# Kernel tuning notes

Measured on AMD Instinct MI355X. Metric: run time of the kernel, lower is better.

Reference implementation:

```python
import jax, jax.numpy as jnp
import numpy as np

B, S, E, L, H, FF, CB = 16, 1000, 512, 4, 8, 2048, 4096
DH = E // H

def _ln(x, g, b):
    m = x.mean(-1, keepdims=True)
    v = ((x - m) ** 2).mean(-1, keepdims=True)
    return (x - m) / jnp.sqrt(v + 1e-5) * g + b

def setup_inputs() -> dict:
    key = jax.random.key(0)
    cnt = [0]
    def rn(shape, s=0.02):
        cnt[0] += 1
        return jax.random.normal(jax.random.fold_in(key, cnt[0]), shape, jnp.float32) * s
    inp = {}
    inp['noisy_tokens'] = jax.random.randint(jax.random.fold_in(key, 999), (B, S), 0, CB, dtype=jnp.int32)
    inp['codebook'] = rn((CB, E), 1.0)
    # sinusoidal positional encoding, as in _create_positional_encoding
    pe = np.zeros((S, E), np.float32)
    pos = np.arange(S, dtype=np.float32)[:, None]
    div = np.exp(np.arange(0, E, 2, dtype=np.float32) * (-np.log(10000.0) / E))
    pe[:, 0::2] = np.sin(pos * div)
    pe[:, 1::2] = np.cos(pos * div)
    inp['pos_enc'] = jnp.asarray(pe)[None]  # [1,S,E]
    # transformer encoder layers (stacked over L)
    inp['qkv_w'] = rn((L, 3 * E, E)); inp['qkv_b'] = jnp.zeros((L, 3 * E))
    inp['out_w'] = rn((L, E, E));     inp['out_b'] = jnp.zeros((L, E))
    inp['ln1_g'] = jnp.ones((L, E));  inp['ln1_b'] = jnp.zeros((L, E))
    inp['ln2_g'] = jnp.ones((L, E));  inp['ln2_b'] = jnp.zeros((L, E))
    inp['ff1_w'] = rn((L, FF, E));    inp['ff1_b'] = jnp.zeros((L, FF))
    inp['ff2_w'] = rn((L, E, FF));    inp['ff2_b'] = jnp.zeros((L, E))
    inp['fin_g'] = jnp.ones((E,));    inp['fin_b'] = jnp.zeros((E,))
    # post_process: Linear, LN, GELU, Linear
    inp['pp1_w'] = rn((E, E)); inp['pp1_b'] = jnp.zeros((E,))
    inp['pp_ln_g'] = jnp.ones((E,)); inp['pp_ln_b'] = jnp.zeros((E,))
    inp['pp2_w'] = rn((E, E)); inp['pp2_b'] = jnp.zeros((E,))
    inp['res_w'] = jnp.float32(0.1)
    # feature_to_codebook: Linear, LN, GELU, Linear (codebook_dim == E)
    inp['fc1_w'] = rn((E, E)); inp['fc1_b'] = jnp.zeros((E,))
    inp['fc_ln_g'] = jnp.ones((E,)); inp['fc_ln_b'] = jnp.zeros((E,))
    inp['fc2_w'] = rn((E, E)); inp['fc2_b'] = jnp.zeros((E,))
    return inp

def reference(noisy_tokens, codebook, pos_enc, qkv_w, qkv_b, out_w, out_b,
              ln1_g, ln1_b, ln2_g, ln2_b, ff1_w, ff1_b, ff2_w, ff2_b,
              fin_g, fin_b, pp1_w, pp1_b, pp_ln_g, pp_ln_b, pp2_w, pp2_b,
              res_w, fc1_w, fc1_b, fc_ln_g, fc_ln_b, fc2_w, fc2_b):
    gelu = lambda z: jax.nn.gelu(z, approximate=False)
    # token embedding (codebook_projection is Identity) + positional encoding
    x = codebook[noisy_tokens] + pos_enc            # [B,S,E]
    # pre-norm transformer encoder (dropout=0 / eval)
    y = x
    for l in range(L):
        h = _ln(y, ln1_g[l], ln1_b[l])
        qkv = h @ qkv_w[l].T + qkv_b[l]             # [B,S,3E]
        q, k, v = jnp.split(qkv, 3, axis=-1)
        q = q.reshape(B, S, H, DH); k = k.reshape(B, S, H, DH); v = v.reshape(B, S, H, DH)
        scores = jnp.einsum('bqhd,bkhd->bhqk', q, k) / jnp.sqrt(jnp.float32(DH))
        attn = jax.nn.softmax(scores, axis=-1)
        ctx = jnp.einsum('bhqk,bkhd->bqhd', attn, v).reshape(B, S, E)
        y = y + (ctx @ out_w[l].T + out_b[l])
        h2 = _ln(y, ln2_g[l], ln2_b[l])
        y = y + (gelu(h2 @ ff1_w[l].T + ff1_b[l]) @ ff2_w[l].T + ff2_b[l])
    y = _ln(y, fin_g, fin_b)
    # post_process + residual
    pp = gelu(_ln(y @ pp1_w.T + pp1_b, pp_ln_g, pp_ln_b)) @ pp2_w.T + pp2_b
    enhanced = x + res_w * pp
    # feature_to_codebook
    fc = gelu(_ln(enhanced @ fc1_w.T + fc1_b, fc_ln_g, fc_ln_b)) @ fc2_w.T + fc2_b  # [B,S,E]
    # quantize: nearest neighbour in codebook (cdist + argmin)
    flat = fc.reshape(-1, E)
    d2 = (jnp.sum(flat ** 2, -1, keepdims=True)
          - 2.0 * flat @ codebook.T
          + jnp.sum(codebook ** 2, -1))            # [B*S, CB]
    tokens = jnp.argmin(d2, axis=-1).reshape(B, S)
    return fc, tokens
```

## Files before the change

### kernel.cpp

```cpp
#include <hip/hip_runtime.h>
#include <hip/hip_bf16.h>
#include <math.h>

#define NTOK 16000
#define E    512
#define FFD  2048
#define CBN  4096
#define SEQ  1000
#define NH   8
#define VLD  1008

typedef __hip_bfloat16 bf16;
typedef __attribute__((ext_vector_type(8))) short short8;
typedef __attribute__((ext_vector_type(4))) float f32x4;

__device__ __forceinline__ float gelu_f(float v) {
    return 0.5f * v * (1.0f + erff(v * 0.70710678118654752f));
}

__device__ __forceinline__ void split_store(float v, bf16* hi, bf16* lo, size_t idx) {
    bf16 h = __float2bfloat16(v);
    hi[idx] = h;
    lo[idx] = __float2bfloat16(v - __bfloat162float(h));
}

__device__ __forceinline__ void t2_ins(float v, int c, float& v1, int& c1, float& v2, int& c2) {
    const bool b1 = (v < v1) || (v == v1 && c < c1);
    const bool b2 = (v < v2) || (v == v2 && c < c2);
    if (b1) { v2 = v1; c2 = c1; v1 = v; c1 = c; }
    else if (b2) { v2 = v; c2 = c; }
}

__global__ __launch_bounds__(128) void embed_kernel(const int* __restrict__ tok,
                                                    const float* __restrict__ cb,
                                                    const float* __restrict__ pe,
                                                    float* __restrict__ y) {
    const int row = blockIdx.x;
    const int s = row % SEQ;
    const int t = tok[row];
    const int c = threadIdx.x * 4;
    const float4 cv = *(const float4*)(cb + (size_t)t * E + c);
    const float4 pv = *(const float4*)(pe + (size_t)s * E + c);
    *(float4*)(y + (size_t)row * E + c) =
        make_float4(cv.x + pv.x, cv.y + pv.y, cv.z + pv.z, cv.w + pv.w);
}

__global__ __launch_bounds__(256) void split_w(const float* __restrict__ src, int ld,
                                               int cols_log2, int n,
                                               bf16* __restrict__ hi, bf16* __restrict__ lo) {
    const int i = blockIdx.x * 256 + threadIdx.x;
    if (i >= n) return;
    const int r = i >> cols_log2;
    const int c = i & ((1 << cols_log2) - 1);
    const float v = src[(size_t)r * ld + c];
    split_store(v, hi, lo, i);
}

template<int GELU>
__global__ __launch_bounds__(256) void ln_planes(const float* __restrict__ in,
                                                 bf16* __restrict__ hi, bf16* __restrict__ lo,
                                                 const float* __restrict__ g,
                                                 const float* __restrict__ b) {
    const int lane = threadIdx.x & 63;
    const int row = blockIdx.x * 4 + (threadIdx.x >> 6);
    const float* p = in + (size_t)row * E;
    const float4 v0 = *(const float4*)(p + lane * 4);
    const float4 v1 = *(const float4*)(p + 256 + lane * 4);
    float sum = v0.x + v0.y + v0.z + v0.w + v1.x + v1.y + v1.z + v1.w;
    float sq = v0.x * v0.x + v0.y * v0.y + v0.z * v0.z + v0.w * v0.w
             + v1.x * v1.x + v1.y * v1.y + v1.z * v1.z + v1.w * v1.w;
#pragma unroll
    for (int m = 1; m < 64; m <<= 1) {
        sum += __shfl_xor(sum, m);
        sq += __shfl_xor(sq, m);
    }
    const float mean = sum * (1.0f / 512.0f);
    const float var = sq * (1.0f / 512.0f) - mean * mean;
    const float rstd = rsqrtf(var + 1e-5f);
    const float4 g0 = *(const float4*)(g + lane * 4);
    const float4 g1 = *(const float4*)(g + 256 + lane * 4);
    const float4 b0 = *(const float4*)(b + lane * 4);
    const float4 b1 = *(const float4*)(b + 256 + lane * 4);
    const size_t base = (size_t)row * E;
    float o;
    const float vv0[4] = {v0.x, v0.y, v0.z, v0.w};
    const float gg0[4] = {g0.x, g0.y, g0.z, g0.w};
    const float bb0[4] = {b0.x, b0.y, b0.z, b0.w};
    const float vv1[4] = {v1.x, v1.y, v1.z, v1.w};
    const float gg1[4] = {g1.x, g1.y, g1.z, g1.w};
    const float bb1[4] = {b1.x, b1.y, b1.z, b1.w};
#pragma unroll
    for (int t = 0; t < 4; ++t) {
        o = (vv0[t] - mean) * rstd * gg0[t] + bb0[t];
        if (GELU) o = gelu_f(o);
        split_store(o, hi, lo, base + lane * 4 + t);
        o = (vv1[t] - mean) * rstd * gg1[t] + bb1[t];
        if (GELU) o = gelu_f(o);
        split_store(o, hi, lo, base + 256 + lane * 4 + t);
    }
}

template<int OUT>
__global__ __launch_bounds__(256) void gemm_split(
    const bf16* __restrict__ Ah, const bf16* __restrict__ Al, int lda,
    const bf16* __restrict__ Wh, const bf16* __restrict__ Wl, int ldw,
    const float* __restrict__ bias,
    float* __restrict__ C, int ldc,
    bf16* __restrict__ Ohi, bf16* __restrict__ Olo, int ldp,
    const int* __restrict__ noisy, const float* __restrict__ cb,
    const float* __restrict__ pe, const float* __restrict__ resw,
    int K) {
    __shared__ short Ash[2][128][40];
    __shared__ short Wsh[2][128][40];
    const int tid = threadIdx.x;
    const int rowBase = blockIdx.y * 128;
    const int colBase = blockIdx.x * 128;
    const int wave = tid >> 6, lane = tid & 63;
    const int wm = (wave & 1) * 64, wn = (wave >> 1) * 64;
    const int lm = lane & 15;
    const int q8 = (lane >> 4) * 8;
    const int r0 = tid >> 2;
    const int kq = (tid & 3) * 8;

    f32x4 acc[4][4];
#pragma unroll
    for (int i = 0; i < 4; ++i)
#pragma unroll
        for (int j = 0; j < 4; ++j)
            acc[i][j] = (f32x4){0.f, 0.f, 0.f, 0.f};

    for (int k0 = 0; k0 < K; k0 += 32) {
        __syncthreads();
        {
            const size_t a0 = (size_t)(rowBase + r0) * lda + k0 + kq;
            const size_t a1 = (size_t)(rowBase + r0 + 64) * lda + k0 + kq;
            const size_t w0 = (size_t)(colBase + r0) * ldw + k0 + kq;
            const size_t w1 = (size_t)(colBase + r0 + 64) * ldw + k0 + kq;
            *(short8*)&Ash[0][r0][kq]      = *(const short8*)(Ah + a0);
            *(short8*)&Ash[0][r0 + 64][kq] = *(const short8*)(Ah + a1);
            *(short8*)&Ash[1][r0][kq]      = *(const short8*)(Al + a0);
            *(short8*)&Ash[1][r0 + 64][kq] = *(const short8*)(Al + a1);
            *(short8*)&Wsh[0][r0][kq]      = *(const short8*)(Wh + w0);
            *(short8*)&Wsh[0][r0 + 64][kq] = *(const short8*)(Wh + w1);
            *(short8*)&Wsh[1][r0][kq]      = *(const short8*)(Wl + w0);
            *(short8*)&Wsh[1][r0 + 64][kq] = *(const short8*)(Wl + w1);
        }
        __syncthreads();
        short8 ah[4], al[4], wh[4], wl[4];
#pragma unroll
        for (int i = 0; i < 4; ++i) {
            ah[i] = *(const short8*)&Ash[0][wm + i * 16 + lm][q8];
            al[i] = *(const short8*)&Ash[1][wm + i * 16 + lm][q8];
            wh[i] = *(const short8*)&Wsh[0][wn + i * 16 + lm][q8];
            wl[i] = *(const short8*)&Wsh[1][wn + i * 16 + lm][q8];
        }
#pragma unroll
        for (int i = 0; i < 4; ++i)
#pragma unroll
            for (int j = 0; j < 4; ++j)
                acc[i][j] = __builtin_amdgcn_mfma_f32_16x16x32_bf16(ah[i], wh[j], acc[i][j], 0, 0, 0);
#pragma unroll
        for (int i = 0; i < 4; ++i)
#pragma unroll
            for (int j = 0; j < 4; ++j)
                acc[i][j] = __builtin_amdgcn_mfma_f32_16x16x32_bf16(ah[i], wl[j], acc[i][j], 0, 0, 0);
#pragma unroll
        for (int i = 0; i < 4; ++i)
#pragma unroll
            for (int j = 0; j < 4; ++j)
                acc[i][j] = __builtin_amdgcn_mfma_f32_16x16x32_bf16(al[i], wh[j], acc[i][j], 0, 0, 0);
    }

    float bv[4];
#pragma unroll
    for (int j = 0; j < 4; ++j)
        bv[j] = bias ? bias[colBase + wn + j * 16 + lm] : 0.f;
    float scv = 0.f;
    if (OUT == 3) scv = resw[0];
#pragma unroll
    for (int i = 0; i < 4; ++i) {
#pragma unroll
        for (int reg = 0; reg < 4; ++reg) {
            const int r = rowBase + wm + i * 16 + (lane >> 4) * 4 + reg;
            int tok = 0, srow = 0;
            if (OUT == 3) { tok = noisy[r]; srow = r % SEQ; }
#pragma unroll
            for (int j = 0; j < 4; ++j) {
                const int col = colBase + wn + j * 16 + lm;
                float v = acc[i][j][reg] + bv[j];
                if (OUT == 0) {
                    C[(size_t)r * ldc + col] = v;
                } else if (OUT == 1) {
                    float* cp = C + (size_t)r * ldc + col;
                    *cp = *cp + v;
                } else if (OUT == 2) {
                    v = gelu_f(v);
                    split_store(v, Ohi, Olo, (size_t)r * ldp + col);
                } else if (OUT == 3) {
                    const float xv = cb[(size_t)tok * E + col] + pe[(size_t)srow * E + col];
                    v = xv + scv * v;
                    split_store(v, Ohi, Olo, (size_t)r * ldp + col);
                } else {
                    split_store(v, Ohi, Olo, (size_t)r * ldp + col);
                }
            }
        }
    }
}

__global__ __launch_bounds__(256) void vtrans(const bf16* __restrict__ vh_src,
                                              const bf16* __restrict__ vl_src,
                                              bf16* __restrict__ vth,
                                              bf16* __restrict__ vtl) {
    __shared__ short T[64][72];
    const int tid = threadIdx.x;
    const int st = blockIdx.x;
    const int bh = blockIdx.y;
    const int b = bh >> 3, h = bh & 7;
    const int sr = tid >> 2, dq = (tid & 3) * 16;
    const int s_g = st * 64 + sr;
    const int od = tid >> 3;
    const int osq = (tid & 7) * 8;
#pragma unroll
    for (int p = 0; p < 2; ++p) {
        const short* src = (const short*)(p ? vl_src : vh_src);
        short* dst = (short*)(p ? vtl : vth);
        short8 a0 = {0, 0, 0, 0, 0, 0, 0, 0};
        short8 a1 = {0, 0, 0, 0, 0, 0, 0, 0};
        if (s_g < SEQ) {
            const short* sp = src + (size_t)(b * SEQ + s_g) * 1536 + 1024 + h * 64 + dq;
            a0 = *(const short8*)sp;
            a1 = *(const short8*)(sp + 8);
        }
        __syncthreads();
#pragma unroll
        for (int j = 0; j < 8; ++j) T[dq + j][sr] = a0[j];
#pragma unroll
        for (int j = 0; j < 8; ++j) T[dq + 8 + j][sr] = a1[j];
        __syncthreads();
        const int scol = st * 64 + osq;
        if (scol + 8 <= VLD) {
            const short8 o0 = *(const short8*)&T[od][osq];
            const short8 o1 = *(const short8*)&T[od + 32][osq];
            *(short8*)(dst + (size_t)(bh * 64 + od) * VLD + scol) = o0;
            *(short8*)(dst + (size_t)(bh * 64 + od + 32) * VLD + scol) = o1;
        }
    }
}

__global__ __launch_bounds__(256) void attn_mfma(const bf16* __restrict__ qkh,
                                                 const bf16* __restrict__ qkl,
                                                 const bf16* __restrict__ vth,
                                                 const bf16* __restrict__ vtl,
                                                 bf16* __restrict__ chi,
                                                 bf16* __restrict__ clo) {
    __shared__ short QPs[2][64][72];
    __shared__ short Ks[2][64][72];
    __shared__ short Vs[2][64][72];
    const int tid = threadIdx.x;
    const int qt = blockIdx.x, bh = blockIdx.y;
    const int b = bh >> 3, h = bh & 7;
    const int wave = tid >> 6, lane = tid & 63;
    const int lm = lane & 15, g = lane >> 4, q8 = g * 8;
    const int wq = wave * 16;
    const int r0 = tid >> 2, kq = (tid & 3) * 16;

    {
        const int q = qt * 64 + r0;
        short8 z = {0, 0, 0, 0, 0, 0, 0, 0};
        short8 a0 = z, a1 = z, b0 = z, b1 = z;
        if (q < SEQ) {
            const size_t base = (size_t)(b * SEQ + q) * 1536 + h * 64 + kq;
            a0 = *(const short8*)((const short*)qkh + base);
            a1 = *(const short8*)((const short*)qkh + base + 8);
            b0 = *(const short8*)((const short*)qkl + base);
            b1 = *(const short8*)((const short*)qkl + base + 8);
        }
        *(short8*)&QPs[0][r0][kq] = a0; *(short8*)&QPs[0][r0][kq + 8] = a1;
        *(short8*)&QPs[1][r0][kq] = b0; *(short8*)&QPs[1][r0][kq + 8] = b1;
    }
    __syncthreads();
    short8 qfh[2], qfl[2];
#pragma unroll
    for (int t = 0; t < 2; ++t) {
        qfh[t] = *(const short8*)&QPs[0][wq + lm][t * 32 + q8];
        qfl[t] = *(const short8*)&QPs[1][wq + lm][t * 32 + q8];
    }

    float m_i[4] = {-3e38f, -3e38f, -3e38f, -3e38f};
    float l_i[4] = {0.f, 0.f, 0.f, 0.f};
    f32x4 o[4];
#pragma unroll
    for (int dt = 0; dt < 4; ++dt) o[dt] = (f32x4){0.f, 0.f, 0.f, 0.f};

    for (int kb = 0; kb < SEQ; kb += 64) {
        __syncthreads();
        {
            const int kr = kb + r0;
            short8 z = {0, 0, 0, 0, 0, 0, 0, 0};
            short8 a0 = z, a1 = z, b0 = z, b1 = z;
            if (kr < SEQ) {
                const size_t base = (size_t)(b * SEQ + kr) * 1536 + 512 + h * 64 + kq;
                a0 = *(const short8*)((const short*)qkh + base);
                a1 = *(const short8*)((const short*)qkh + base + 8);
                b0 = *(const short8*)((const short*)qkl + base);
                b1 = *(const short8*)((const short*)qkl + base + 8);
            }
            *(short8*)&Ks[0][r0][kq] = a0; *(short8*)&Ks[0][r0][kq + 8] = a1;
            *(short8*)&Ks[1][r0][kq] = b0; *(short8*)&Ks[1][r0][kq + 8] = b1;
            const size_t vbase = (size_t)(bh * 64 + r0) * VLD + kb + kq;
            short8 v0 = z, v1 = z, w0 = z, w1 = z;
            if (kb + kq + 8 <= VLD) {
                v0 = *(const short8*)((const short*)vth + vbase);
                w0 = *(const short8*)((const short*)vtl + vbase);
            }
            if (kb + kq + 16 <= VLD) {
                v1 = *(const short8*)((const short*)vth + vbase + 8);
                w1 = *(const short8*)((const short*)vtl + vbase + 8);
            }
            *(short8*)&Vs[0][r0][kq] = v0; *(short8*)&Vs[0][r0][kq + 8] = v1;
            *(short8*)&Vs[1][r0][kq] = w0; *(short8*)&Vs[1][r0][kq + 8] = w1;
        }
        __syncthreads();
        f32x4 sac[4];
#pragma unroll
        for (int j = 0; j < 4; ++j) sac[j] = (f32x4){0.f, 0.f, 0.f, 0.f};
#pragma unroll
        for (int t = 0; t < 2; ++t) {
#pragma unroll
            for (int j = 0; j < 4; ++j) {
                const short8 kh = *(const short8*)&Ks[0][j * 16 + lm][t * 32 + q8];
                const short8 kl = *(const short8*)&Ks[1][j * 16 + lm][t * 32 + q8];
                sac[j] = __builtin_amdgcn_mfma_f32_16x16x32_bf16(qfh[t], kh, sac[j], 0, 0, 0);
                sac[j] = __builtin_amdgcn_mfma_f32_16x16x32_bf16(qfh[t], kl, sac[j], 0, 0, 0);
                sac[j] = __builtin_amdgcn_mfma_f32_16x16x32_bf16(qfl[t], kh, sac[j], 0, 0, 0);
            }
        }
        float alpha_v[4];
#pragma unroll
        for (int reg = 0; reg < 4; ++reg) {
            float sv[4];
            float rm = -3e38f;
#pragma unroll
            for (int j = 0; j < 4; ++j) {
                const int kc = kb + j * 16 + lm;
                float s = sac[j][reg] * 0.125f;
                s = (kc < SEQ) ? s : -3e38f;
                sv[j] = s;
                rm = fmaxf(rm, s);
            }
#pragma unroll
            for (int m = 1; m < 16; m <<= 1) rm = fmaxf(rm, __shfl_xor(rm, m));
            const float mn = fmaxf(m_i[reg], rm);
            const float al = expf(m_i[reg] - mn);
            float rs = 0.f;
            const int prow = wq + g * 4 + reg;
#pragma unroll
            for (int j = 0; j < 4; ++j) {
                const float pv = expf(sv[j] - mn);
                rs += pv;
                bf16 phb = __float2bfloat16(pv);
                bf16 plb = __float2bfloat16(pv - __bfloat162float(phb));
                QPs[0][prow][j * 16 + lm] = *reinterpret_cast<short*>(&phb);
                QPs[1][prow][j * 16 + lm] = *reinterpret_cast<short*>(&plb);
            }
#pragma unroll
            for (int m = 1; m < 16; m <<= 1) rs += __shfl_xor(rs, m);
            l_i[reg] = l_i[reg] * al + rs;
            m_i[reg] = mn;
            alpha_v[reg] = al;
        }
        const f32x4 av = {alpha_v[0], alpha_v[1], alpha_v[2], alpha_v[3]};
#pragma unroll
        for (int dt = 0; dt < 4; ++dt) o[dt] *= av;
        __syncthreads();
#pragma unroll
        for (int t = 0; t < 2; ++t) {
            const short8 ph = *(const short8*)&QPs[0][wq + lm][t * 32 + q8];
            const short8 pl = *(const short8*)&QPs[1][wq + lm][t * 32 + q8];
#pragma unroll
            for (int dt = 0; dt < 4; ++dt) {
                const short8 vh = *(const short8*)&Vs[0][dt * 16 + lm][t * 32 + q8];
                const short8 vl = *(const short8*)&Vs[1][dt * 16 + lm][t * 32 + q8];
                o[dt] = __builtin_amdgcn_mfma_f32_16x16x32_bf16(ph, vh, o[dt], 0, 0, 0);
                o[dt] = __builtin_amdgcn_mfma_f32_16x16x32_bf16(ph, vl, o[dt], 0, 0, 0);
                o[dt] = __builtin_amdgcn_mfma_f32_16x16x32_bf16(pl, vh, o[dt], 0, 0, 0);
            }
        }
    }
#pragma unroll
    for (int reg = 0; reg < 4; ++reg) {
        const int q = qt * 64 + wq + g * 4 + reg;
        if (q < SEQ) {
            const float inv = 1.0f / l_i[reg];
#pragma unroll
            for (int dt = 0; dt < 4; ++dt) {
                const size_t idx = (size_t)(b * SEQ + q) * E + h * 64 + dt * 16 + lm;
                split_store(o[dt][reg] * inv, chi, clo, idx);
            }
        }
    }
}

__global__ __launch_bounds__(256) void cbnorm_kernel(const float* __restrict__ cb,
                                                     float* __restrict__ out) {
    const int lane = threadIdx.x & 63;
    const int row = blockIdx.x * 4 + (threadIdx.x >> 6);
    const float* p = cb + (size_t)row * E;
    const float4 v0 = *(const float4*)(p + lane * 4);
    const float4 v1 = *(const float4*)(p + 256 + lane * 4);
    float sq = v0.x * v0.x + v0.y * v0.y + v0.z * v0.z + v0.w * v0.w
             + v1.x * v1.x + v1.y * v1.y + v1.z * v1.z + v1.w * v1.w;
#pragma unroll
    for (int m = 1; m < 64; m <<= 1) sq += __shfl_xor(sq, m);
    if (lane == 0) out[row] = sq;
}

__global__ __launch_bounds__(256) void argmin_mfma(
    const bf16* __restrict__ Ah, const bf16* __restrict__ Al,
    const bf16* __restrict__ Wh, const bf16* __restrict__ Wl,
    const float* __restrict__ cbn, float4* __restrict__ part) {
    __shared__ short Ash[2][128][40];
    __shared__ short Wsh[2][128][40];
    const int tid = threadIdx.x;
    const int rowBase = blockIdx.y * 128;
    const int colBase = blockIdx.x * 128;
    const int wave = tid >> 6, lane = tid & 63;
    const int wm = (wave & 1) * 64, wn = (wave >> 1) * 64;
    const int lm = lane & 15;
    const int q8 = (lane >> 4) * 8;
    const int r0 = tid >> 2;
    const int kq = (tid & 3) * 8;

    f32x4 acc[4][4];
#pragma unroll
    for (int i = 0; i < 4; ++i)
#pragma unroll
        for (int j = 0; j < 4; ++j)
            acc[i][j] = (f32x4){0.f, 0.f, 0.f, 0.f};

    for (int k0 = 0; k0 < E; k0 += 32) {
        __syncthreads();
        {
            const size_t a0 = (size_t)(rowBase + r0) * E + k0 + kq;
            const size_t a1 = (size_t)(rowBase + r0 + 64) * E + k0 + kq;
            const size_t w0 = (size_t)(colBase + r0) * E + k0 + kq;
            const size_t w1 = (size_t)(colBase + r0 + 64) * E + k0 + kq;
            *(short8*)&Ash[0][r0][kq]      = *(const short8*)(Ah + a0);
            *(short8*)&Ash[0][r0 + 64][kq] = *(const short8*)(Ah + a1);
            *(short8*)&Ash[1][r0][kq]      = *(const short8*)(Al + a0);
            *(short8*)&Ash[1][r0 + 64][kq] = *(const short8*)(Al + a1);
            *(short8*)&Wsh[0][r0][kq]      = *(const short8*)(Wh + w0);
            *(short8*)&Wsh[0][r0 + 64][kq] = *(const short8*)(Wh + w1);
            *(short8*)&Wsh[1][r0][kq]      = *(const short8*)(Wl + w0);
            *(short8*)&Wsh[1][r0 + 64][kq] = *(const short8*)(Wl + w1);
        }
        __syncthreads();
        short8 ah[4], al[4], wh[4], wl[4];
#pragma unroll
        for (int i = 0; i < 4; ++i) {
            ah[i] = *(const short8*)&Ash[0][wm + i * 16 + lm][q8];
            al[i] = *(const short8*)&Ash[1][wm + i * 16 + lm][q8];
            wh[i] = *(const short8*)&Wsh[0][wn + i * 16 + lm][q8];
            wl[i] = *(const short8*)&Wsh[1][wn + i * 16 + lm][q8];
        }
#pragma unroll
        for (int i = 0; i < 4; ++i)
#pragma unroll
            for (int j = 0; j < 4; ++j)
                acc[i][j] = __builtin_amdgcn_mfma_f32_16x16x32_bf16(ah[i], wh[j], acc[i][j], 0, 0, 0);
#pragma unroll
        for (int i = 0; i < 4; ++i)
#pragma unroll
            for (int j = 0; j < 4; ++j)
                acc[i][j] = __builtin_amdgcn_mfma_f32_16x16x32_bf16(ah[i], wl[j], acc[i][j], 0, 0, 0);
#pragma unroll
        for (int i = 0; i < 4; ++i)
#pragma unroll
            for (int j = 0; j < 4; ++j)
                acc[i][j] = __builtin_amdgcn_mfma_f32_16x16x32_bf16(al[i], wh[j], acc[i][j], 0, 0, 0);
    }

    float nv[4];
#pragma unroll
    for (int j = 0; j < 4; ++j) nv[j] = cbn[colBase + wn + j * 16 + lm];
    const int hx = blockIdx.x * 2 + (wn >> 6);
#pragma unroll
    for (int i = 0; i < 4; ++i) {
#pragma unroll
        for (int reg = 0; reg < 4; ++reg) {
            const int r = rowBase + wm + i * 16 + (lane >> 4) * 4 + reg;
            float v1 = 3e38f, v2 = 3e38f;
            int c1 = 0x7fffffff, c2 = 0x7fffffff;
#pragma unroll
            for (int j = 0; j < 4; ++j) {
                const int col = colBase + wn + j * 16 + lm;
                const float d = nv[j] - 2.0f * acc[i][j][reg];
                t2_ins(d, col, v1, c1, v2, c2);
            }
#pragma unroll
            for (int m = 1; m < 16; m <<= 1) {
                const float w1 = __shfl_xor(v1, m); const int d1 = __shfl_xor(c1, m);
                const float w2 = __shfl_xor(v2, m); const int d2 = __shfl_xor(c2, m);
                t2_ins(w1, d1, v1, c1, v2, c2);
                t2_ins(w2, d2, v1, c1, v2, c2);
            }
            if (lm == 0)
                part[(size_t)r * 64 + hx] = make_float4(v1, (float)c1, v2, (float)c2);
        }
    }
}

__global__ __launch_bounds__(256) void argmin_exact(const float4* __restrict__ part,
                                                    const float* __restrict__ fc,
                                                    const float* __restrict__ cb,
                                                    const float* __restrict__ cbn,
                                                    float* __restrict__ tokf) {
    const int wave = threadIdx.x >> 6, lane = threadIdx.x & 63;
    const int r = blockIdx.x * 4 + wave;
    const float4 p = part[(size_t)r * 64 + lane];
    float v1 = p.x, v2 = p.z;
    int c1 = (int)p.y, c2 = (int)p.w;
#pragma unroll
    for (int m = 1; m < 64; m <<= 1) {
        const float w1 = __shfl_xor(v1, m); const int d1 = __shfl_xor(c1, m);
        const float w2 = __shfl_xor(v2, m); const int d2 = __shfl_xor(c2, m);
        t2_ins(w1, d1, v1, c1, v2, c2);
        t2_ins(w2, d2, v1, c1, v2, c2);
    }
    const float* fr = fc + (size_t)r * E + lane * 8;
    const float* p1 = cb + (size_t)c1 * E + lane * 8;
    const float* p2 = cb + (size_t)c2 * E + lane * 8;
    float d1 = 0.f, d2 = 0.f;
#pragma unroll
    for (int j = 0; j < 8; ++j) {
        const float f = fr[j];
        d1 += f * p1[j];
        d2 += f * p2[j];
    }
#pragma unroll
    for (int m = 1; m < 64; m <<= 1) {
        d1 += __shfl_xor(d1, m);
        d2 += __shfl_xor(d2, m);
    }
    d1 = cbn[c1] - 2.0f * d1;
    d2 = cbn[c2] - 2.0f * d2;
    const int win = ((d1 < d2) || (d1 == d2 && c1 < c2)) ? c1 : c2;
    if (lane == 0) tokf[r] = (float)win;
}

extern "C" void kernel_launch(void* const* d_in, const int* in_sizes, int n_in,
                              void* d_out, int out_size, void* d_ws, size_t ws_size,
                              hipStream_t stream) {
    const int* noisy = (const int*)d_in[0];
    const float* codebook = (const float*)d_in[1];
    const float* pos_enc = (const float*)d_in[2];
    const float* qkv_w = (const float*)d_in[3];
    const float* qkv_b = (const float*)d_in[4];
    const float* out_w = (const float*)d_in[5];
    const float* out_b = (const float*)d_in[6];
    const float* ln1_g = (const float*)d_in[7];
    const float* ln1_b = (const float*)d_in[8];
    const float* ln2_g = (const float*)d_in[9];
    const float* ln2_b = (const float*)d_in[10];
    const float* ff1_w = (const float*)d_in[11];
    const float* ff1_b = (const float*)d_in[12];
    const float* ff2_w = (const float*)d_in[13];
    const float* ff2_b = (const float*)d_in[14];
    const float* fin_g = (const float*)d_in[15];
    const float* fin_b = (const float*)d_in[16];
    const float* pp1_w = (const float*)d_in[17];
    const float* pp1_b = (const float*)d_in[18];
    const float* pp_ln_g = (const float*)d_in[19];
    const float* pp_ln_b = (const float*)d_in[20];
    const float* pp2_w = (const float*)d_in[21];
    const float* pp2_b = (const float*)d_in[22];
    const float* res_w = (const float*)d_in[23];
    const float* fc1_w = (const float*)d_in[24];
    const float* fc1_b = (const float*)d_in[25];
    const float* fc_ln_g = (const float*)d_in[26];
    const float* fc_ln_b = (const float*)d_in[27];
    const float* fc2_w = (const float*)d_in[28];
    const float* fc2_b = (const float*)d_in[29];

    float* ws = (float*)d_ws;
    float* y = ws;
    float* REG = ws + 8192000;
    bf16* qkvh = (bf16*)REG;
    bf16* qkvl = qkvh + 24576000;
    bf16* mid_hi = (bf16*)REG;
    bf16* mid_lo = mid_hi + 16384000;
    float* slotA = REG;
    float* slotB = REG + 8192000;
    bf16* e_hi = (bf16*)slotA;
    bf16* e_lo = e_hi + 8192000;
    float* WV = ws + 32768000;
    bf16* vth = (bf16*)WV;
    bf16* vtl = vth + 8192 * VLD;
    bf16* wA_hi = (bf16*)WV;
    bf16* wA_lo = wA_hi + 1048576;
    bf16* wB_hi = wA_lo + 1048576;
    bf16* wB_lo = wB_hi + 1048576;
    bf16* cbh = wB_lo + 1048576;
    bf16* cbl = cbh + 2097152;
    float* cbn = slotB;
    float4* part = (float4*)(slotB + 4096);
    bf16* h_hi = (bf16*)d_out;
    bf16* h_lo = h_hi + 8192000;
    bf16* fcp_hi = (bf16*)d_out;
    bf16* fcp_lo = fcp_hi + 8192000;
    float* tokf = (float*)d_out + 8192000;

    const dim3 blk(256);
    const dim3 g512(4, 125), g1024(8, 125), g1536(12, 125);

    embed_kernel<<<dim3(NTOK), dim3(128), 0, stream>>>(noisy, codebook, pos_enc, y);

    for (int l = 0; l < 4; ++l) {
        ln_planes<0><<<dim3(4000), blk, 0, stream>>>(y, h_hi, h_lo, ln1_g + l * E, ln1_b + l * E);
        split_w<<<dim3(3072), blk, 0, stream>>>(qkv_w + (size_t)l * 1536 * E, E, 9, 1536 * E, wA_hi, wA_lo);
        gemm_split<4><<<g1536, blk, 0, stream>>>(
            h_hi, h_lo, E, wA_hi, wA_lo, E, qkv_b + (size_t)l * 1536,
            nullptr, 0, qkvh, qkvl, 1536, nullptr, nullptr, nullptr, nullptr, E);
        vtrans<<<dim3(16, 128), blk, 0, stream>>>(qkvh, qkvl, vth, vtl);
        attn_mfma<<<dim3(16, 128), blk, 0, stream>>>(qkvh, qkvl, vth, vtl, h_hi, h_lo);
        split_w<<<dim3(1024), blk, 0, stream>>>(out_w + (size_t)l * E * E, E, 9, E * E, wB_hi, wB_lo);
        gemm_split<1><<<g512, blk, 0, stream>>>(
            h_hi, h_lo, E, wB_hi, wB_lo, E, out_b + (size_t)l * E,
            y, E, nullptr, nullptr, 0, nullptr, nullptr, nullptr, nullptr, E);
        ln_planes<0><<<dim3(4000), blk, 0, stream>>>(y, h_hi, h_lo, ln2_g + l * E, ln2_b + l * E);
        split_w<<<dim3(4096), blk, 0, stream>>>(ff1_w + (size_t)l * FFD * E, E, 9, FFD * E, wA_hi, wA_lo);
        split_w<<<dim3(4096), blk, 0, stream>>>(ff2_w + (size_t)l * E * FFD, FFD, 11, E * FFD, wB_hi, wB_lo);
        for (int c = 0; c < 2; ++c) {
            gemm_split<2><<<g1024, blk, 0, stream>>>(
                h_hi, h_lo, E, wA_hi + (size_t)c * 1024 * E, wA_lo + (size_t)c * 1024 * E, E,
                ff1_b + (size_t)l * FFD + c * 1024,
                nullptr, 0, mid_hi, mid_lo, 1024, nullptr, nullptr, nullptr, nullptr, E);
            gemm_split<1><<<g512, blk, 0, stream>>>(
                mid_hi, mid_lo, 1024, wB_hi + c * 1024, wB_lo + c * 1024, FFD,
                (c == 0) ? (ff2_b + (size_t)l * E) : nullptr,
                y, E, nullptr, nullptr, 0, nullptr, nullptr, nullptr, nullptr, 1024);
        }
    }

    ln_planes<0><<<dim3(4000), blk, 0, stream>>>(y, h_hi, h_lo, fin_g, fin_b);
    split_w<<<dim3(1024), blk, 0, stream>>>(pp1_w, E, 9, E * E, wA_hi, wA_lo);
    gemm_split<0><<<g512, blk, 0, stream>>>(
        h_hi, h_lo, E, wA_hi, wA_lo, E, pp1_b,
        slotB, E, nullptr, nullptr, 0, nullptr, nullptr, nullptr, nullptr, E);
    ln_planes<1><<<dim3(4000), blk, 0, stream>>>(slotB, h_hi, h_lo, pp_ln_g, pp_ln_b);
    split_w<<<dim3(1024), blk, 0, stream>>>(pp2_w, E, 9, E * E, wB_hi, wB_lo);
    gemm_split<3><<<g512, blk, 0, stream>>>(
        h_hi, h_lo, E, wB_hi, wB_lo, E, pp2_b,
        nullptr, 0, e_hi, e_lo, E, noisy, codebook, pos_enc, res_w, E);
    split_w<<<dim3(1024), blk, 0, stream>>>(fc1_w, E, 9, E * E, wA_hi, wA_lo);
    gemm_split<0><<<g512, blk, 0, stream>>>(
        e_hi, e_lo, E, wA_hi, wA_lo, E, fc1_b,
        slotB, E, nullptr, nullptr, 0, nullptr, nullptr, nullptr, nullptr, E);
    ln_planes<1><<<dim3(4000), blk, 0, stream>>>(slotB, h_hi, h_lo, fc_ln_g, fc_ln_b);
    split_w<<<dim3(1024), blk, 0, stream>>>(fc2_w, E, 9, E * E, wB_hi, wB_lo);
    gemm_split<0><<<g512, blk, 0, stream>>>(
        h_hi, h_lo, E, wB_hi, wB_lo, E, fc2_b,
        slotA, E, nullptr, nullptr, 0, nullptr, nullptr, nullptr, nullptr, E);

    split_w<<<dim3(32000), blk, 0, stream>>>(slotA, E, 9, NTOK * E, fcp_hi, fcp_lo);
    split_w<<<dim3(8192), blk, 0, stream>>>(codebook, E, 9, CBN * E, cbh, cbl);
    cbnorm_kernel<<<dim3(1024), blk, 0, stream>>>(codebook, cbn);
    argmin_mfma<<<dim3(32, 125), blk, 0, stream>>>(fcp_hi, fcp_lo, cbh, cbl, cbn, part);
    argmin_exact<<<dim3(4000), blk, 0, stream>>>(part, slotA, codebook, cbn, tokf);
    hipMemcpyAsync(d_out, slotA, (size_t)8192000 * 4, hipMemcpyDeviceToDevice, stream);
}
```

Measured before the change: 4.233 ms.

## Loop argmin blocks over four codebook tiles and merge top-2 in LDS

Each argmin block now sweeps 512 codebook columns in four 128-column tiles and keeps a running top-2 per row. Each wave owns 32 rows across all 128 columns, and partial results are merged through shared memory instead of shuffle reductions. This cuts the partial-result buffer from 64 to 8 entries per row, which simplifies the exact-argmin pass. It also changes the wave tiling: more B-fragment LDS reads per wave, and four times fewer blocks (1000 instead of 4000).

```diff
diff --git a/kernel.cpp b/kernel.cpp
--- a/kernel.cpp
+++ b/kernel.cpp
@@ -420,95 +420,117 @@
     const bf16* __restrict__ Ah, const bf16* __restrict__ Al,
     const bf16* __restrict__ Wh, const bf16* __restrict__ Wl,
     const float* __restrict__ cbn, float4* __restrict__ part) {
-    __shared__ short Ash[2][128][40];
-    __shared__ short Wsh[2][128][40];
+    __shared__ __align__(16) short sbuf[2][2][128][40];
+    float4* mrg = reinterpret_cast<float4*>(&sbuf[0][0][0][0]);
     const int tid = threadIdx.x;
     const int rowBase = blockIdx.y * 128;
-    const int colBase = blockIdx.x * 128;
     const int wave = tid >> 6, lane = tid & 63;
-    const int wm = (wave & 1) * 64, wn = (wave >> 1) * 64;
+    const int wm = wave * 32;
     const int lm = lane & 15;
-    const int q8 = (lane >> 4) * 8;
+    const int g = lane >> 4;
+    const int q8 = g * 8;
     const int r0 = tid >> 2;
     const int kq = (tid & 3) * 8;
-
-    f32x4 acc[4][4];
-#pragma unroll
-    for (int i = 0; i < 4; ++i)
-#pragma unroll
-        for (int j = 0; j < 4; ++j)
-            acc[i][j] = (f32x4){0.f, 0.f, 0.f, 0.f};
-
-    for (int k0 = 0; k0 < E; k0 += 32) {
+    const int own_row = tid >> 1;
+    const int own_half = tid & 1;
+
+    float rv1 = 3e38f, rv2 = 3e38f;
+    int rc1 = 0x7fffffff, rc2 = 0x7fffffff;
+
+    for (int ct = 0; ct < 4; ++ct) {
+        const int colBase = blockIdx.x * 512 + ct * 128;
+        f32x4 acc[2][8];
+#pragma unroll
+        for (int i = 0; i < 2; ++i)
+#pragma unroll
+            for (int j = 0; j < 8; ++j)
+                acc[i][j] = (f32x4){0.f, 0.f, 0.f, 0.f};
+
+        for (int k0 = 0; k0 < E; k0 += 32) {
+            __syncthreads();
+            {
+                const size_t a0 = (size_t)(rowBase + r0) * E + k0 + kq;
+                const size_t a1 = (size_t)(rowBase + r0 + 64) * E + k0 + kq;
+                const size_t w0 = (size_t)(colBase + r0) * E + k0 + kq;
+                const size_t w1 = (size_t)(colBase + r0 + 64) * E + k0 + kq;
+                *(short8*)&sbuf[0][0][r0][kq]      = *(const short8*)(Ah + a0);
+                *(short8*)&sbuf[0][0][r0 + 64][kq] = *(const short8*)(Ah + a1);
+                *(short8*)&sbuf[0][1][r0][kq]      = *(const short8*)(Al + a0);
+                *(short8*)&sbuf[0][1][r0 + 64][kq] = *(const short8*)(Al + a1);
+                *(short8*)&sbuf[1][0][r0][kq]      = *(const short8*)(Wh + w0);
+                *(short8*)&sbuf[1][0][r0 + 64][kq] = *(const short8*)(Wh + w1);
+                *(short8*)&sbuf[1][1][r0][kq]      = *(const short8*)(Wl + w0);
+                *(short8*)&sbuf[1][1][r0 + 64][kq] = *(const short8*)(Wl + w1);
+            }
+            __syncthreads();
+            short8 ah[2], al2[2], wh[8], wl[8];
+#pragma unroll
+            for (int i = 0; i < 2; ++i) {
+                ah[i]  = *(const short8*)&sbuf[0][0][wm + i * 16 + lm][q8];
+                al2[i] = *(const short8*)&sbuf[0][1][wm + i * 16 + lm][q8];
+            }
+#pragma unroll
+            for (int j = 0; j < 8; ++j) {
+                wh[j] = *(const short8*)&sbuf[1][0][j * 16 + lm][q8];
+                wl[j] = *(const short8*)&sbuf[1][1][j * 16 + lm][q8];
+            }
+#pragma unroll
+            for (int i = 0; i < 2; ++i)
+#pragma unroll
+                for (int j = 0; j < 8; ++j)
+                    acc[i][j] = __builtin_amdgcn_mfma_f32_16x16x32_bf16(ah[i], wh[j], acc[i][j], 0, 0, 0);
+#pragma unroll
+            for (int i = 0; i < 2; ++i)
+#pragma unroll
+                for (int j = 0; j < 8; ++j)
+                    acc[i][j] = __builtin_amdgcn_mfma_f32_16x16x32_bf16(ah[i], wl[j], acc[i][j], 0, 0, 0);
+#pragma unroll
+            for (int i = 0; i < 2; ++i)
+#pragma unroll
+                for (int j = 0; j < 8; ++j)
+                    acc[i][j] = __builtin_amdgcn_mfma_f32_16x16x32_bf16(al2[i], wh[j], acc[i][j], 0, 0, 0);
+        }
+
+        float nv[8];
+#pragma unroll
+        for (int j = 0; j < 8; ++j) nv[j] = cbn[colBase + j * 16 + lm];
+        __syncthreads();
+#pragma unroll
+        for (int i = 0; i < 2; ++i) {
+#pragma unroll
+            for (int reg = 0; reg < 4; ++reg) {
+                const int row_local = wm + i * 16 + g * 4 + reg;
+                float v1 = 3e38f, v2 = 3e38f;
+                int c1 = 0x7fffffff, c2 = 0x7fffffff;
+#pragma unroll
+                for (int j = 0; j < 8; ++j) {
+                    const float d = nv[j] - 2.0f * acc[i][j][reg];
+                    t2_ins(d, colBase + j * 16 + lm, v1, c1, v2, c2);
+                }
+                mrg[row_local * 17 + lm] = make_float4(v1, (float)c1, v2, (float)c2);
+            }
+        }
         __syncthreads();
         {
-            const size_t a0 = (size_t)(rowBase + r0) * E + k0 + kq;
-            const size_t a1 = (size_t)(rowBase + r0 + 64) * E + k0 + kq;
-            const size_t w0 = (size_t)(colBase + r0) * E + k0 + kq;
-            const size_t w1 = (size_t)(colBase + r0 + 64) * E + k0 + kq;
-            *(short8*)&Ash[0][r0][kq]      = *(const short8*)(Ah + a0);
-            *(short8*)&Ash[0][r0 + 64][kq] = *(const short8*)(Ah + a1);
-            *(short8*)&Ash[1][r0][kq]      = *(const short8*)(Al + a0);
-            *(short8*)&Ash[1][r0 + 64][kq] = *(const short8*)(Al + a1);
-            *(short8*)&Wsh[0][r0][kq]      = *(const short8*)(Wh + w0);
-            *(short8*)&Wsh[0][r0 + 64][kq] = *(const short8*)(Wh + w1);
-            *(short8*)&Wsh[1][r0][kq]      = *(const short8*)(Wl + w0);
-            *(short8*)&Wsh[1][r0 + 64][kq] = *(const short8*)(Wl + w1);
-        }
-        __syncthreads();
-        short8 ah[4], al[4], wh[4], wl[4];
-#pragma unroll
-        for (int i = 0; i < 4; ++i) {
-            ah[i] = *(const short8*)&Ash[0][wm + i * 16 + lm][q8];
-            al[i] = *(const short8*)&Ash[1][wm + i * 16 + lm][q8];
-            wh[i] = *(const short8*)&Wsh[0][wn + i * 16 + lm][q8];
-            wl[i] = *(const short8*)&Wsh[1][wn + i * 16 + lm][q8];
-        }
-#pragma unroll
-        for (int i = 0; i < 4; ++i)
-#pragma unroll
-            for (int j = 0; j < 4; ++j)
-                acc[i][j] = __builtin_amdgcn_mfma_f32_16x16x32_bf16(ah[i], wh[j], acc[i][j], 0, 0, 0);
-#pragma unroll
-        for (int i = 0; i < 4; ++i)
-#pragma unroll
-            for (int j = 0; j < 4; ++j)
-                acc[i][j] = __builtin_amdgcn_mfma_f32_16x16x32_bf16(ah[i], wl[j], acc[i][j], 0, 0, 0);
-#pragma unroll
-        for (int i = 0; i < 4; ++i)
-#pragma unroll
-            for (int j = 0; j < 4; ++j)
-                acc[i][j] = __builtin_amdgcn_mfma_f32_16x16x32_bf16(al[i], wh[j], acc[i][j], 0, 0, 0);
-    }
-
-    float nv[4];
-#pragma unroll
-    for (int j = 0; j < 4; ++j) nv[j] = cbn[colBase + wn + j * 16 + lm];
-    const int hx = blockIdx.x * 2 + (wn >> 6);
-#pragma unroll
-    for (int i = 0; i < 4; ++i) {
-#pragma unroll
-        for (int reg = 0; reg < 4; ++reg) {
-            const int r = rowBase + wm + i * 16 + (lane >> 4) * 4 + reg;
-            float v1 = 3e38f, v2 = 3e38f;
-            int c1 = 0x7fffffff, c2 = 0x7fffffff;
-#pragma unroll
-            for (int j = 0; j < 4; ++j) {
-                const int col = colBase + wn + j * 16 + lm;
-                const float d = nv[j] - 2.0f * acc[i][j][reg];
-                t2_ins(d, col, v1, c1, v2, c2);
-            }
-#pragma unroll
-            for (int m = 1; m < 16; m <<= 1) {
-                const float w1 = __shfl_xor(v1, m); const int d1 = __shfl_xor(c1, m);
-                const float w2 = __shfl_xor(v2, m); const int d2 = __shfl_xor(c2, m);
-                t2_ins(w1, d1, v1, c1, v2, c2);
-                t2_ins(w2, d2, v1, c1, v2, c2);
-            }
-            if (lm == 0)
-                part[(size_t)r * 64 + hx] = make_float4(v1, (float)c1, v2, (float)c2);
-        }
-    }
+            float mv1 = 3e38f, mv2 = 3e38f;
+            int mc1 = 0x7fffffff, mc2 = 0x7fffffff;
+#pragma unroll
+            for (int e = 0; e < 8; ++e) {
+                const float4 p = mrg[own_row * 17 + own_half * 8 + e];
+                t2_ins(p.x, (int)p.y, mv1, mc1, mv2, mc2);
+                t2_ins(p.z, (int)p.w, mv1, mc1, mv2, mc2);
+            }
+            const float pv1 = __shfl_xor(mv1, 1); const int pc1 = __shfl_xor(mc1, 1);
+            const float pv2 = __shfl_xor(mv2, 1); const int pc2 = __shfl_xor(mc2, 1);
+            t2_ins(pv1, pc1, mv1, mc1, mv2, mc2);
+            t2_ins(pv2, pc2, mv1, mc1, mv2, mc2);
+            t2_ins(mv1, mc1, rv1, rc1, rv2, rc2);
+            t2_ins(mv2, mc2, rv1, rc1, rv2, rc2);
+        }
+    }
+    if (own_half == 0)
+        part[(size_t)(rowBase + own_row) * 8 + blockIdx.x] =
+            make_float4(rv1, (float)rc1, rv2, (float)rc2);
 }
 
 __global__ __launch_bounds__(256) void argmin_exact(const float4* __restrict__ part,
@@ -518,16 +540,21 @@
                                                     float* __restrict__ tokf) {
     const int wave = threadIdx.x >> 6, lane = threadIdx.x & 63;
     const int r = blockIdx.x * 4 + wave;
-    const float4 p = part[(size_t)r * 64 + lane];
-    float v1 = p.x, v2 = p.z;
-    int c1 = (int)p.y, c2 = (int)p.w;
-#pragma unroll
-    for (int m = 1; m < 64; m <<= 1) {
-        const float w1 = __shfl_xor(v1, m); const int d1 = __shfl_xor(c1, m);
-        const float w2 = __shfl_xor(v2, m); const int d2 = __shfl_xor(c2, m);
-        t2_ins(w1, d1, v1, c1, v2, c2);
-        t2_ins(w2, d2, v1, c1, v2, c2);
-    }
+    float v1 = 3e38f, v2 = 3e38f;
+    int c1 = 0x7fffffff, c2 = 0x7fffffff;
+    if (lane < 8) {
+        const float4 p = part[(size_t)r * 8 + lane];
+        v1 = p.x; c1 = (int)p.y; v2 = p.z; c2 = (int)p.w;
+    }
+#pragma unroll
+    for (int m = 1; m < 8; m <<= 1) {
+        const float w1 = __shfl_xor(v1, m); const int d1i = __shfl_xor(c1, m);
+        const float w2 = __shfl_xor(v2, m); const int d2i = __shfl_xor(c2, m);
+        t2_ins(w1, d1i, v1, c1, v2, c2);
+        t2_ins(w2, d2i, v1, c1, v2, c2);
+    }
+    c1 = __shfl(c1, 0);
+    c2 = __shfl(c2, 0);
     const float* fr = fc + (size_t)r * E + lane * 8;
     const float* p1 = cb + (size_t)c1 * E + lane * 8;
     const float* p2 = cb + (size_t)c2 * E + lane * 8;
@@ -666,7 +693,7 @@
     split_w<<<dim3(32000), blk, 0, stream>>>(slotA, E, 9, NTOK * E, fcp_hi, fcp_lo);
     split_w<<<dim3(8192), blk, 0, stream>>>(codebook, E, 9, CBN * E, cbh, cbl);
     cbnorm_kernel<<<dim3(1024), blk, 0, stream>>>(codebook, cbn);
-    argmin_mfma<<<dim3(32, 125), blk, 0, stream>>>(fcp_hi, fcp_lo, cbh, cbl, cbn, part);
+    argmin_mfma<<<dim3(8, 125), blk, 0, stream>>>(fcp_hi, fcp_lo, cbh, cbl, cbn, part);
     argmin_exact<<<dim3(4000), blk, 0, stream>>>(part, slotA, codebook, cbn, tokf);
     hipMemcpyAsync(d_out, slotA, (size_t)8192000 * 4, hipMemcpyDeviceToDevice, stream);
 }
```

Measured after the change: 3.819 ms. -9.8%, faster.
